# Kernel tuning notes

Measured on AMD Instinct MI355X. Metric: run time of the kernel, lower is better.

The kernel has to match this reference:

```python
import jax, jax.numpy as jnp
import numpy as np

DEPTH = 8
IN_FEATURES = 512
OUT_FEATURES = 64
BATCH = 4096
LEAF_COUNT = 2 ** DEPTH          # 256
GATE_COUNT = LEAF_COUNT - 1      # 255


def tree_paths(depth):
    """Replicates the torch loop: for each leaf i, the gate index visited at each
    level j and whether the path takes the right branch (bit '1' -> 1-gating)."""
    leaves = 2 ** depth
    idx = np.zeros((depth, leaves), dtype=np.int32)
    bit = np.zeros((depth, leaves), dtype=bool)
    for i in range(leaves):
        bits = np.binary_repr(i, width=depth)
        index = 1
        for j in range(depth):
            idx[j, i] = index - 1
            bit[j, i] = (bits[j] == '1')
            index = 2 * index + (1 if bits[j] == '1' else 0)
    return idx, bit


def setup_inputs() -> dict:
    key = jax.random.key(0)
    kx, kg, kp = jax.random.split(key, 3)
    x = jax.random.normal(kx, (BATCH, IN_FEATURES), dtype=jnp.float32)
    # kaiming_normal_(nonlinearity='sigmoid') on [gate_count, in_features]: gain=1,
    # fan_in = in_features -> std = 1/sqrt(in_features); stored transposed.
    gw = jax.random.normal(kg, (IN_FEATURES, GATE_COUNT), dtype=jnp.float32) / np.sqrt(IN_FEATURES)
    gb = jnp.zeros((GATE_COUNT,), dtype=jnp.float32)
    # kaiming_normal_(nonlinearity='linear') on [out*leaf, in]: std = 1/sqrt(in_features),
    # reshaped to [out, leaf, in] then permuted to [out, in, leaf].
    pw = jax.random.normal(kp, (OUT_FEATURES, IN_FEATURES, LEAF_COUNT), dtype=jnp.float32) / np.sqrt(IN_FEATURES)
    pb = jnp.zeros((OUT_FEATURES, LEAF_COUNT), dtype=jnp.float32)
    idx, bit = tree_paths(DEPTH)
    return {
        'x': x, 'gw': gw, 'gb': gb, 'pw': pw, 'pb': pb,
        'leaf_idx': jnp.asarray(idx), 'leaf_bit': jnp.asarray(bit),
    }


def reference(x, gw, gb, pw, pb, leaf_idx, leaf_bit):
    # gatings: [B, gate_count]
    gatings = jax.nn.sigmoid(x @ gw + gb)
    # gather gate prob along each leaf path: [B, depth, leaf_count]
    g_sel = gatings[:, leaf_idx]
    branch = jnp.where(leaf_bit[None], 1.0 - g_sel, g_sel)
    leaf_probs = jnp.prod(branch, axis=1)            # [B, leaf_count]
    # per-leaf projection of x, plus bias: [B, out, leaf_count]
    per_leaf = jnp.einsum('bi,oil->bol', x, pw) + pb[None]
    # mixture over leaves: [B, out]
    return jnp.einsum('bol,bl->bo', per_leaf, leaf_probs)
```

## Files before the change

kernel.cpp:

```cpp
#include <hip/hip_runtime.h>
#include <cstdint>
#include <cstddef>

#define GATES 255

typedef __attribute__((ext_vector_type(8))) short bf16x8;
typedef __attribute__((ext_vector_type(4))) float f32x4;

__device__ __forceinline__ short f2bf(float f) {
  union { float f; uint32_t u; } c; c.f = f;
  uint32_t r = c.u + 0x7FFFu + ((c.u >> 16) & 1u);
  return (short)(r >> 16);
}

#define GLOAD16(gp, lp) __builtin_amdgcn_global_load_lds( \
    (const __attribute__((address_space(1))) uint32_t*)(gp), \
    (__attribute__((address_space(3))) uint32_t*)(lp), 16, 0, 0)

__global__ __launch_bounds__(256) void k_prep(const float* __restrict__ x,
                                              short* __restrict__ xb,
                                              const float* __restrict__ gw,
                                              short* __restrict__ gwt,
                                              const float* __restrict__ pw,
                                              short* __restrict__ pwt) {
  __shared__ short t[64][65];
  const int bx = blockIdx.x;
  const int tid = threadIdx.x;

  if (bx < 2048) {
    const int i = bx * 256 + tid;
    const float4 v = ((const float4*)x)[i];
    short4 s;
    s.x = f2bf(v.x); s.y = f2bf(v.y); s.z = f2bf(v.z); s.w = f2bf(v.w);
    ((short4*)xb)[i] = s;
    return;
  }

  const int c = tid & 63, r0 = tid >> 6;

  if (bx < 2080) {
    const int b2 = bx - 2048;
    const int ib = b2 >> 2, gb = b2 & 3;
    const int i0 = ib << 6, g0 = gb << 6;
#pragma unroll
    for (int rr = 0; rr < 16; ++rr) {
      const int i = rr * 4 + r0;
      const int g = g0 + c;
      t[i][c] = (g < GATES) ? f2bf(gw[(size_t)(i0 + i) * GATES + g]) : (short)0;
    }
    __syncthreads();
#pragma unroll
    for (int rr = 0; rr < 16; ++rr) {
      const int gg = rr * 4 + r0;
      gwt[(size_t)(g0 + gg) * 512 + i0 + c] = t[c][gg];
    }
    return;
  }

  const int b2 = bx - 2080;
  const int o = b2 >> 5;
  const int ib = (b2 >> 2) & 7;
  const int lb = b2 & 3;
  const int i0 = ib << 6, l0 = lb << 6;
  const float* src = pw + ((size_t)o * 512 + i0) * 256 + l0;
#pragma unroll
  for (int rr = 0; rr < 16; ++rr) {
    const int i = rr * 4 + r0;
    t[i][c] = f2bf(src[(size_t)i * 256 + c]);
  }
  __syncthreads();
  short* dst = pwt + ((size_t)o * 256 + l0) * 512 + i0;
#pragma unroll
  for (int rr = 0; rr < 16; ++rr) {
    const int ll = rr * 4 + r0;
    dst[(size_t)ll * 512 + c] = t[c][ll];
  }
}

__global__ __launch_bounds__(256, 1) void k_gate(const short* __restrict__ xb,
                                                 const short* __restrict__ gwt,
                                                 const float* __restrict__ gb,
                                                 float* __restrict__ p) {
  __shared__ short a_lds[32 * 64];
  __shared__ short b_lds[256 * 64];
  __shared__ float gs[32][260];

  const int b0 = blockIdx.x << 5;
  const int tid = threadIdx.x;
  const int lane = tid & 63;
  const int w = tid >> 6;
  const int wr = w >> 1, wc = w & 1;

  const short* Ab = xb + (size_t)b0 * 512;

  f32x4 acc[8];
#pragma unroll
  for (int nf = 0; nf < 8; ++nf) {
    acc[nf][0] = 0.f; acc[nf][1] = 0.f; acc[nf][2] = 0.f; acc[nf][3] = 0.f;
  }

  for (int s = 0; s < 8; ++s) {
    const int i0 = s << 6;
    __syncthreads();
    {
      const int c = tid;
      const int r = c >> 3, cc = (c & 7) << 3;
      GLOAD16(Ab + (size_t)r * 512 + i0 + cc, a_lds + c * 8);
    }
#pragma unroll
    for (int sw = 0; sw < 8; ++sw) {
      const int chunk = sw * 256 + tid;
      const int r = chunk >> 3, cc = (chunk & 7) << 3;
      GLOAD16(gwt + (size_t)r * 512 + i0 + cc, b_lds + chunk * 8);
    }
    __syncthreads();
#pragma unroll
    for (int kk = 0; kk < 2; ++kk) {
      const int kb = (kk << 5) + ((lane >> 4) << 3);
      bf16x8 af, bfr[8];
      {
        const int row = (wr << 4) + (lane & 15);
        af = *(const bf16x8*)(a_lds + row * 64 + kb);
      }
#pragma unroll
      for (int nf = 0; nf < 8; ++nf) {
        const int row = (wc << 7) + (nf << 4) + (lane & 15);
        bfr[nf] = *(const bf16x8*)(b_lds + row * 64 + kb);
      }
#pragma unroll
      for (int nf = 0; nf < 8; ++nf)
        acc[nf] = __builtin_amdgcn_mfma_f32_16x16x32_bf16(
            af, bfr[nf], acc[nf], 0, 0, 0);
    }
  }

  const int grp = lane >> 4, lcol = lane & 15;
#pragma unroll
  for (int nf = 0; nf < 8; ++nf) {
    const int g = (wc << 7) + (nf << 4) + lcol;
    const float bias = (g < GATES) ? gb[g] : 0.f;
#pragma unroll
    for (int rg = 0; rg < 4; ++rg) {
      const int bl = (wr << 4) + (grp << 2) + rg;
      const float z = acc[nf][rg] + bias;
      gs[bl][g] = 1.f / (1.f + __expf(-z));
    }
  }
  __syncthreads();

  const int l = tid;
  for (int r = 0; r < 32; ++r) {
    float prob = 1.f;
    int index = 1;
#pragma unroll
    for (int j = 0; j < 8; ++j) {
      const int bit = (l >> (7 - j)) & 1;
      const float gg = gs[r][index - 1];
      prob *= bit ? (1.f - gg) : gg;
      index = 2 * index + bit;
    }
    p[(size_t)(b0 + r) * 256 + l] = prob;
  }
}

__global__ __launch_bounds__(512, 4) void k_main(const short* __restrict__ xb,
                                                 const short* __restrict__ pwt,
                                                 const float* __restrict__ p,
                                                 const float* __restrict__ pb,
                                                 float* __restrict__ out) {
  __shared__ short a_lds[128 * 64];
  __shared__ short b_lds[256 * 64];

  const int bx = blockIdx.x;
  const int o = bx >> 5;
  const int bm0 = (bx & 31) << 7;
  const int tid = threadIdx.x;
  const int lane = tid & 63;
  const int w = tid >> 6;
  const int wr = w >> 2;
  const int wc = w & 3;

  const short* Ab = xb + (size_t)bm0 * 512;
  const short* Bb = pwt + (size_t)o * (256 * 512);

  f32x4 acc[4][4];
#pragma unroll
  for (int mf = 0; mf < 4; ++mf)
#pragma unroll
    for (int nf = 0; nf < 4; ++nf) {
      acc[mf][nf][0] = 0.f; acc[mf][nf][1] = 0.f;
      acc[mf][nf][2] = 0.f; acc[mf][nf][3] = 0.f;
    }

  for (int s = 0; s < 8; ++s) {
    const int i0 = s << 6;
    __syncthreads();
#pragma unroll
    for (int j = 0; j < 2; ++j) {
      const int c = j * 512 + tid;
      const int r = c >> 3;
      const int gblk = (c & 7) ^ (r & 7);
      GLOAD16(Ab + (size_t)r * 512 + i0 + (gblk << 3), a_lds + c * 8);
    }
#pragma unroll
    for (int j = 0; j < 4; ++j) {
      const int c = j * 512 + tid;
      const int r = c >> 3;
      const int gblk = (c & 7) ^ (r & 7);
      GLOAD16(Bb + (size_t)r * 512 + i0 + (gblk << 3), b_lds + c * 8);
    }
    __syncthreads();
#pragma unroll
    for (int kk = 0; kk < 2; ++kk) {
      const int kblk = (kk << 2) + (lane >> 4);
      bf16x8 af[4], bfr[4];
#pragma unroll
      for (int mf = 0; mf < 4; ++mf) {
        const int row = (wr << 6) + (mf << 4) + (lane & 15);
        af[mf] = *(const bf16x8*)(a_lds + row * 64 + ((kblk ^ (row & 7)) << 3));
      }
#pragma unroll
      for (int nf = 0; nf < 4; ++nf) {
        const int row = (wc << 6) + (nf << 4) + (lane & 15);
        bfr[nf] = *(const bf16x8*)(b_lds + row * 64 + ((kblk ^ (row & 7)) << 3));
      }
#pragma unroll
      for (int mf = 0; mf < 4; ++mf)
#pragma unroll
        for (int nf = 0; nf < 4; ++nf)
          acc[mf][nf] = __builtin_amdgcn_mfma_f32_16x16x32_bf16(
              af[mf], bfr[nf], acc[mf][nf], 0, 0, 0);
    }
  }

  __syncthreads();
  float* red = (float*)a_lds;
  const int grp = lane >> 4;
  const int lcol = lane & 15;
  float pbv[4];
#pragma unroll
  for (int nf = 0; nf < 4; ++nf)
    pbv[nf] = pb[(size_t)o * 256 + (wc << 6) + (nf << 4) + lcol];
#pragma unroll
  for (int mf = 0; mf < 4; ++mf) {
#pragma unroll
    for (int rg = 0; rg < 4; ++rg) {
      const int bl = (wr << 6) + (mf << 4) + (grp << 2) + rg;
      const int b = bm0 + bl;
      float v = 0.f;
#pragma unroll
      for (int nf = 0; nf < 4; ++nf) {
        const int l = (wc << 6) + (nf << 4) + lcol;
        v += (acc[mf][nf][rg] + pbv[nf]) * p[(size_t)b * 256 + l];
      }
      v += __shfl_xor(v, 1);
      v += __shfl_xor(v, 2);
      v += __shfl_xor(v, 4);
      v += __shfl_xor(v, 8);
      if (lcol == 0) red[wc * 128 + bl] = v;
    }
  }
  __syncthreads();
  if (tid < 128) {
    out[(size_t)(bm0 + tid) * 64 + o] =
        red[tid] + red[128 + tid] + red[256 + tid] + red[384 + tid];
  }
}

extern "C" void kernel_launch(void* const* d_in, const int* in_sizes, int n_in,
                              void* d_out, int out_size, void* d_ws, size_t ws_size,
                              hipStream_t stream) {
  (void)in_sizes; (void)n_in; (void)out_size; (void)ws_size;
  const float* x  = (const float*)d_in[0];
  const float* gw = (const float*)d_in[1];
  const float* gb = (const float*)d_in[2];
  const float* pw = (const float*)d_in[3];
  const float* pb = (const float*)d_in[4];
  float* out = (float*)d_out;

  char* ws = (char*)d_ws;
  short* xbuf = (short*)(ws);
  short* gwt  = (short*)(ws + ((size_t)4 << 20));
  short* pwt  = (short*)(ws + ((size_t)4 << 20) + (256 << 10));
  float* p    = (float*)(ws + ((size_t)20 << 20) + (256 << 10));

  k_prep<<<4128, 256, 0, stream>>>(x, xbuf, gw, gwt, pw, pwt);
  k_gate<<<128, 256, 0, stream>>>(xbuf, gwt, gb, p);
  k_main<<<2048, 512, 0, stream>>>(xbuf, pwt, p, pb, out);
}
```

Measured before the change: 111.4 us.

## Use 4-wave blocks with 64x128 warp tiles and permuted leaf-prob layout

Main GEMM blocks drop from 8 waves to 4, and each wave now computes a 64x128 tile (4x8 MFMA fragments). This reuses each A fragment across more B fragments and halves the cross-wave reduction. The gate kernel now stores leaf probabilities in a permuted order, so the epilogue can fetch the 8 needed probabilities with two float4 loads instead of scattered scalar loads. In exchange, each thread holds more accumulator registers, which lowers occupancy, and each thread issues more async LDS loads per stage.

Result: slower. 113.9 us (+2.2%).

```diff
diff --git a/kernel.cpp b/kernel.cpp
--- a/kernel.cpp
+++ b/kernel.cpp
@@ -148,7 +148,7 @@
   }
   __syncthreads();
 
-  const int l = tid;
+  const int l = ((tid & 15) << 4) | (tid >> 4);
   for (int r = 0; r < 32; ++r) {
     float prob = 1.f;
     int index = 1;
@@ -159,11 +159,11 @@
       prob *= bit ? (1.f - gg) : gg;
       index = 2 * index + bit;
     }
-    p[(size_t)(b0 + r) * 256 + l] = prob;
-  }
-}
-
-__global__ __launch_bounds__(512, 4) void k_main(const short* __restrict__ xb,
+    p[(size_t)(b0 + r) * 256 + tid] = prob;
+  }
+}
+
+__global__ __launch_bounds__(256, 2) void k_main(const short* __restrict__ xb,
                                                  const short* __restrict__ pwt,
                                                  const float* __restrict__ p,
                                                  const float* __restrict__ pb,
@@ -177,17 +177,17 @@
   const int tid = threadIdx.x;
   const int lane = tid & 63;
   const int w = tid >> 6;
-  const int wr = w >> 2;
-  const int wc = w & 3;
+  const int wr = w >> 1;
+  const int wc = w & 1;
 
   const short* Ab = xb + (size_t)bm0 * 512;
   const short* Bb = pwt + (size_t)o * (256 * 512);
 
-  f32x4 acc[4][4];
+  f32x4 acc[4][8];
 #pragma unroll
   for (int mf = 0; mf < 4; ++mf)
 #pragma unroll
-    for (int nf = 0; nf < 4; ++nf) {
+    for (int nf = 0; nf < 8; ++nf) {
       acc[mf][nf][0] = 0.f; acc[mf][nf][1] = 0.f;
       acc[mf][nf][2] = 0.f; acc[mf][nf][3] = 0.f;
     }
@@ -196,15 +196,15 @@
     const int i0 = s << 6;
     __syncthreads();
 #pragma unroll
-    for (int j = 0; j < 2; ++j) {
-      const int c = j * 512 + tid;
+    for (int sw = 0; sw < 4; ++sw) {
+      const int c = sw * 256 + tid;
       const int r = c >> 3;
       const int gblk = (c & 7) ^ (r & 7);
       GLOAD16(Ab + (size_t)r * 512 + i0 + (gblk << 3), a_lds + c * 8);
     }
 #pragma unroll
-    for (int j = 0; j < 4; ++j) {
-      const int c = j * 512 + tid;
+    for (int sw = 0; sw < 8; ++sw) {
+      const int c = sw * 256 + tid;
       const int r = c >> 3;
       const int gblk = (c & 7) ^ (r & 7);
       GLOAD16(Bb + (size_t)r * 512 + i0 + (gblk << 3), b_lds + c * 8);
@@ -213,21 +213,21 @@
 #pragma unroll
     for (int kk = 0; kk < 2; ++kk) {
       const int kblk = (kk << 2) + (lane >> 4);
-      bf16x8 af[4], bfr[4];
+      bf16x8 af[4], bfr[8];
 #pragma unroll
       for (int mf = 0; mf < 4; ++mf) {
         const int row = (wr << 6) + (mf << 4) + (lane & 15);
         af[mf] = *(const bf16x8*)(a_lds + row * 64 + ((kblk ^ (row & 7)) << 3));
       }
 #pragma unroll
-      for (int nf = 0; nf < 4; ++nf) {
-        const int row = (wc << 6) + (nf << 4) + (lane & 15);
+      for (int nf = 0; nf < 8; ++nf) {
+        const int row = (wc << 7) + (nf << 4) + (lane & 15);
         bfr[nf] = *(const bf16x8*)(b_lds + row * 64 + ((kblk ^ (row & 7)) << 3));
       }
 #pragma unroll
       for (int mf = 0; mf < 4; ++mf)
 #pragma unroll
-        for (int nf = 0; nf < 4; ++nf)
+        for (int nf = 0; nf < 8; ++nf)
           acc[mf][nf] = __builtin_amdgcn_mfma_f32_16x16x32_bf16(
               af[mf], bfr[nf], acc[mf][nf], 0, 0, 0);
     }
@@ -237,22 +237,27 @@
   float* red = (float*)a_lds;
   const int grp = lane >> 4;
   const int lcol = lane & 15;
-  float pbv[4];
-#pragma unroll
-  for (int nf = 0; nf < 4; ++nf)
-    pbv[nf] = pb[(size_t)o * 256 + (wc << 6) + (nf << 4) + lcol];
+  float pbv[8];
+#pragma unroll
+  for (int nf = 0; nf < 8; ++nf)
+    pbv[nf] = pb[(size_t)o * 256 + (wc << 7) + (nf << 4) + lcol];
 #pragma unroll
   for (int mf = 0; mf < 4; ++mf) {
 #pragma unroll
     for (int rg = 0; rg < 4; ++rg) {
       const int bl = (wr << 6) + (mf << 4) + (grp << 2) + rg;
       const int b = bm0 + bl;
-      float v = 0.f;
-#pragma unroll
-      for (int nf = 0; nf < 4; ++nf) {
-        const int l = (wc << 6) + (nf << 4) + lcol;
-        v += (acc[mf][nf][rg] + pbv[nf]) * p[(size_t)b * 256 + l];
-      }
+      const float4* pp =
+          (const float4*)(p + (size_t)b * 256 + lcol * 16 + (wc << 3));
+      const float4 p0 = pp[0], p1 = pp[1];
+      float v = (acc[mf][0][rg] + pbv[0]) * p0.x
+              + (acc[mf][1][rg] + pbv[1]) * p0.y
+              + (acc[mf][2][rg] + pbv[2]) * p0.z
+              + (acc[mf][3][rg] + pbv[3]) * p0.w
+              + (acc[mf][4][rg] + pbv[4]) * p1.x
+              + (acc[mf][5][rg] + pbv[5]) * p1.y
+              + (acc[mf][6][rg] + pbv[6]) * p1.z
+              + (acc[mf][7][rg] + pbv[7]) * p1.w;
       v += __shfl_xor(v, 1);
       v += __shfl_xor(v, 2);
       v += __shfl_xor(v, 4);
@@ -262,8 +267,7 @@
   }
   __syncthreads();
   if (tid < 128) {
-    out[(size_t)(bm0 + tid) * 64 + o] =
-        red[tid] + red[128 + tid] + red[256 + tid] + red[384 + tid];
+    out[(size_t)(bm0 + tid) * 64 + o] = red[tid] + red[128 + tid];
   }
 }
 
@@ -286,5 +290,5 @@
 
   k_prep<<<4128, 256, 0, stream>>>(x, xbuf, gw, gwt, pw, pwt);
   k_gate<<<128, 256, 0, stream>>>(xbuf, gwt, gb, p);
-  k_main<<<2048, 512, 0, stream>>>(xbuf, pwt, p, pb, out);
-}
+  k_main<<<2048, 256, 0, stream>>>(xbuf, pwt, p, pb, out);
+}
```
